# Performance work log

Hardware: AMD Instinct MI355X
Metric: run time of the kernel (lower is better)

## Reference

```python
import jax, jax.numpy as jnp
import numpy as np

LOCAL_RADIUS = 127          # block_len = 128
TOKENS_PER_BLOCK = 16       # global_seq_len = L // 16
NEG = -1e9


def _concat_3_blocks(x):
    # x: [B, nb, bl, H, d] -> [B, nb, 3*bl, H, d] (prev, cur, next block; zero-padded ends)
    p = jnp.pad(x, [(0, 0), (1, 1), (0, 0), (0, 0), (0, 0)])
    return jnp.concatenate([p[:, :-2], p[:, 1:-1], p[:, 2:]], axis=2)


def _softmax_with_extra_logit(x, axis=-1):
    m = jnp.maximum(jax.lax.stop_gradient(x.max(axis, keepdims=True)), 0)
    unnorm = jnp.exp(x - m)
    denom = unnorm.sum(axis, keepdims=True) + jnp.exp(-m)
    return unnorm / denom


def setup_inputs() -> dict:
    key = jax.random.key(0)
    ks = jax.random.split(key, 5)
    B, L, D, H, dh = 2, 4096, 1024, 16, 64
    return {
        "x": jax.random.normal(ks[0], (B, L, D), jnp.float32),
        "Wq": jax.random.normal(ks[1], (D, H, dh), jnp.float32) * 0.02,
        "Wk": jax.random.normal(ks[2], (D, H, dh), jnp.float32) * 0.02,
        "Wv": jax.random.normal(ks[3], (D, H, dh), jnp.float32) * 0.02,
        "Wo": jax.random.normal(ks[4], (H, dh, D), jnp.float32) * 0.02,
    }


def reference(x, Wq, Wk, Wv, Wo):
    B, L, D = x.shape
    H, dh = Wq.shape[1], Wq.shape[2]
    bl = LOCAL_RADIUS + 1                      # block_len = 128
    nb = L // bl                               # num_blocks
    G = L // TOKENS_PER_BLOCK                  # global (side) seq len

    q = jnp.einsum("bld,dhk->blhk", x, Wq) / jnp.sqrt(jnp.asarray(dh, x.dtype))
    k = jnp.einsum("bld,dhk->blhk", x, Wk)
    v = jnp.einsum("bld,dhk->blhk", x, Wv)

    # transient-global aggregates: sum token embeddings within each block of TOKENS_PER_BLOCK
    block_ids = jnp.arange(L) // TOKENS_PER_BLOCK          # [L]
    one_hot = jax.nn.one_hot(block_ids, G, dtype=x.dtype)  # [L, G]
    g = jnp.einsum("bld,lg->bgd", x, one_hot)              # [B, G, D]
    side_k = jnp.einsum("bgd,dhk->bghk", g, Wk)
    side_v = jnp.einsum("bgd,dhk->bghk", g, Wv)

    # split into blocks and build 3-block sliding window keys/values
    qb = q.reshape(B, nb, bl, H, dh)
    kb = _concat_3_blocks(k.reshape(B, nb, bl, H, dh))     # [B, nb, 3bl, H, dh]
    vb = _concat_3_blocks(v.reshape(B, nb, bl, H, dh))

    k_cat = jnp.concatenate(
        [kb, jnp.broadcast_to(side_k[:, None], (B, nb, G, H, dh))], axis=2)
    v_cat = jnp.concatenate(
        [vb, jnp.broadcast_to(side_v[:, None], (B, nb, G, H, dh))], axis=2)

    # logits: [B, nb, H, bl, 3bl+G]
    logits = jnp.einsum("bnqhd,bnkhd->bnhqk", qb, k_cat)

    # local mask: enforce |rel| <= local_radius and in-bounds key positions
    q_idx = jnp.arange(bl)[:, None]                        # [bl, 1]
    k_idx = jnp.arange(3 * bl)[None, :]                    # [1, 3bl]
    rel = k_idx - bl - q_idx                               # relative position
    b_idx = jnp.arange(nb)[:, None, None]                  # [nb, 1, 1]
    k_pos = (b_idx - 1) * bl + k_idx                       # absolute key position
    valid = (jnp.abs(rel) <= LOCAL_RADIUS) & (k_pos >= 0) & (k_pos < L)
    local_bias = jnp.where(valid, 0.0, NEG).astype(logits.dtype)  # [nb, bl, 3bl]
    side_bias = jnp.zeros((nb, bl, G), logits.dtype)
    bias = jnp.concatenate([local_bias, side_bias], axis=-1)      # [nb, bl, 3bl+G]
    logits = logits + bias[None, :, None]

    probs = _softmax_with_extra_logit(logits, axis=-1)
    y = jnp.einsum("bnhqk,bnkhd->bnqhd", probs, v_cat)
    y = y.reshape(B, L, H, dh)
    return jnp.einsum("blhk,hkd->bld", y, Wo)
```

## Files before the change

kernel.cpp:

```cpp
#include <hip/hip_runtime.h>
#include <stdint.h>

#define SC_LOG2E 0.18033688011112042f

typedef __attribute__((ext_vector_type(8))) short short8;
typedef __attribute__((ext_vector_type(4))) float f32x4;

__device__ __forceinline__ unsigned short f2bf(float f) {
  unsigned int u = __float_as_uint(f);
  u += 0x7fffu + ((u >> 16) & 1u);
  return (unsigned short)(u >> 16);
}

__device__ __forceinline__ void gload_lds16(const void* g, void* l) {
  __builtin_amdgcn_global_load_lds((const __attribute__((address_space(1))) void*)g,
                                   (__attribute__((address_space(3))) void*)l,
                                   16, 0, 0);
}

__device__ __forceinline__ f32x4 mfma16(short8 a, short8 b, f32x4 c) {
  return __builtin_amdgcn_mfma_f32_16x16x32_bf16(a, b, c, 0, 0, 0);
}


__global__ __launch_bounds__(256) void prep_x_k(const float* __restrict__ x,
                                                unsigned short* __restrict__ xb,
                                                unsigned short* __restrict__ gb) {
  int gr = blockIdx.x;
  int c4 = threadIdx.x;
  const float4* p = (const float4*)(x + (size_t)gr * 16384) + c4;
  float4 s = {0.f, 0.f, 0.f, 0.f};
#pragma unroll
  for (int t = 0; t < 16; ++t) {
    float4 v = p[(size_t)t * 256];
    ushort4 o;
    o.x = f2bf(v.x); o.y = f2bf(v.y); o.z = f2bf(v.z); o.w = f2bf(v.w);
    ((ushort4*)xb)[(size_t)(gr * 16 + t) * 256 + c4] = o;
    s.x += v.x; s.y += v.y; s.z += v.z; s.w += v.w;
  }
  ushort4 og;
  og.x = f2bf(s.x); og.y = f2bf(s.y); og.z = f2bf(s.z); og.w = f2bf(s.w);
  ((ushort4*)gb)[(size_t)gr * 256 + c4] = og;
}

__global__ __launch_bounds__(256) void transpose_w4_k(
    const float* __restrict__ wq, const float* __restrict__ wk,
    const float* __restrict__ wv, const float* __restrict__ wo,
    unsigned short* __restrict__ wqkv_t, unsigned short* __restrict__ wo_t) {
  __shared__ float tile[64 * 65];
  int z = blockIdx.z;
  const float* src = (z == 0) ? wq : (z == 1) ? wk : (z == 2) ? wv : wo;
  unsigned short* dst = (z == 3) ? wo_t : (wqkv_t + (size_t)z * 1048576);
  float scale = (z == 0) ? SC_LOG2E : 1.0f;
  int tc = blockIdx.x * 64, tr = blockIdx.y * 64;
  int cx = threadIdx.x & 63, ry = threadIdx.x >> 6;
#pragma unroll
  for (int i = 0; i < 16; ++i) {
    int r = ry + i * 4;
    tile[r * 65 + cx] = src[(size_t)(tr + r) * 1024 + tc + cx];
  }
  __syncthreads();
#pragma unroll
  for (int i = 0; i < 16; ++i) {
    int r = ry + i * 4;
    dst[(size_t)(tc + r) * 1024 + tr + cx] = f2bf(tile[cx * 65 + r] * scale);
  }
}

__global__ __launch_bounds__(256) void transpose_bf16_k(
    const unsigned short* __restrict__ src, int sstride, size_t szstride,
    unsigned short* __restrict__ dst, int dstride, size_t dzstride) {
  __shared__ unsigned short tile[64 * 65];
  src += blockIdx.z * szstride;
  dst += blockIdx.z * dzstride;
  int tc = blockIdx.x * 64, tr = blockIdx.y * 64;
  int cx = threadIdx.x & 63, ry = threadIdx.x >> 6;
#pragma unroll
  for (int i = 0; i < 16; ++i) {
    int r = ry + i * 4;
    tile[r * 65 + cx] = src[(size_t)(tr + r) * sstride + tc + cx];
  }
  __syncthreads();
#pragma unroll
  for (int i = 0; i < 16; ++i) {
    int r = ry + i * 4;
    dst[(size_t)(tc + r) * dstride + tr + cx] = tile[cx * 65 + r];
  }
}

__global__ __launch_bounds__(512, 2) void gemm256_k(
    const unsigned short* __restrict__ A, const unsigned short* __restrict__ Bt,
    unsigned short* __restrict__ C, int M, int N, int K, int nbn) {
  __shared__ unsigned short lds[2][2][16384];
  int nwg = gridDim.x, cpx = nwg >> 3;
  int bid = blockIdx.x;
  bid = (bid & 7) * cpx + (bid >> 3);
  int bm = bid / nbn, bn = bid % nbn;
  int lane = threadIdx.x & 63, w = threadIdx.x >> 6;
  int wm = w >> 2, wn = w & 3;
  int l15 = lane & 15, lg = lane >> 4;
  int lrow = lane >> 3;
  int lcol = ((lane & 7) ^ lrow) * 8;
  const int KT = K >> 6;

  const unsigned short* Ab = A + ((size_t)bm * 256 + lrow) * K + lcol;
  const unsigned short* Bb = Bt + ((size_t)bn * 256 + lrow) * K + lcol;

  f32x4 zero4 = {0.f, 0.f, 0.f, 0.f};
  f32x4 acc[8][4];
#pragma unroll
  for (int i = 0; i < 8; ++i)
#pragma unroll
    for (int j = 0; j < 4; ++j) acc[i][j] = zero4;

  auto stage = [&](int kind, int t) {
    if (t >= KT) return;
    const unsigned short* src = (kind < 2) ? Ab : Bb;
#pragma unroll
    for (int i = 0; i < 2; ++i) {
      int q = i * 64 + w * 8;
      int r0;
      if (kind == 0)      r0 = (q & 63) + ((q >> 6) << 7);
      else if (kind == 1) r0 = (q & 63) + ((q >> 6) << 7) + 64;
      else if (kind == 2) r0 = (q & 31) + ((q >> 5) << 6);
      else                r0 = (q & 31) + ((q >> 5) << 6) + 32;
      gload_lds16(src + (size_t)r0 * K + t * 64,
                  &lds[t & 1][kind < 2 ? 0 : 1][r0 * 64]);
    }
  };
  auto ldA = [&](int p, int mi, int kk) -> short8 {
    int r = wm * 128 + mi * 16 + l15;
    return *(const short8*)&lds[p][0][r * 64 + ((kk * 32 + lg * 8) ^ ((r & 7) * 8))];
  };
  auto ldB = [&](int p, int ni, int kk) -> short8 {
    int r = wn * 64 + ni * 16 + l15;
    return *(const short8*)&lds[p][1][r * 64 + ((kk * 32 + lg * 8) ^ ((r & 7) * 8))];
  };

  stage(0, 0); stage(3, 0); stage(1, 0); stage(2, 0);
  stage(0, 1); stage(3, 1); stage(1, 1);
  asm volatile("s_waitcnt vmcnt(6)" ::: "memory");
  __builtin_amdgcn_s_barrier();

  for (int t = 0; t < KT; ++t) {
    int p = t & 1;
    short8 aF[4][2], b0[2][2], b1[2][2];
#pragma unroll
    for (int mi = 0; mi < 4; ++mi)
#pragma unroll
      for (int kk = 0; kk < 2; ++kk) aF[mi][kk] = ldA(p, mi, kk);
#pragma unroll
    for (int ni = 0; ni < 2; ++ni)
#pragma unroll
      for (int kk = 0; kk < 2; ++kk) b0[ni][kk] = ldB(p, ni, kk);
    stage(2, t + 1);
    __builtin_amdgcn_s_barrier();
    __builtin_amdgcn_s_setprio(1);
#pragma unroll
    for (int mi = 0; mi < 4; ++mi)
#pragma unroll
      for (int ni = 0; ni < 2; ++ni)
#pragma unroll
        for (int kk = 0; kk < 2; ++kk)
          acc[mi][ni] = mfma16(aF[mi][kk], b0[ni][kk], acc[mi][ni]);
    __builtin_amdgcn_s_setprio(0);
    __builtin_amdgcn_s_barrier();
#pragma unroll
    for (int ni = 0; ni < 2; ++ni)
#pragma unroll
      for (int kk = 0; kk < 2; ++kk) b1[ni][kk] = ldB(p, ni + 2, kk);
    stage(0, t + 2);
    __builtin_amdgcn_s_barrier();
    __builtin_amdgcn_s_setprio(1);
#pragma unroll
    for (int mi = 0; mi < 4; ++mi)
#pragma unroll
      for (int ni = 0; ni < 2; ++ni)
#pragma unroll
        for (int kk = 0; kk < 2; ++kk)
          acc[mi][ni + 2] = mfma16(aF[mi][kk], b1[ni][kk], acc[mi][ni + 2]);
    __builtin_amdgcn_s_setprio(0);
    __builtin_amdgcn_s_barrier();
#pragma unroll
    for (int mi = 0; mi < 4; ++mi)
#pragma unroll
      for (int kk = 0; kk < 2; ++kk) aF[mi][kk] = ldA(p, mi + 4, kk);
    stage(3, t + 2);
    __builtin_amdgcn_s_barrier();
    __builtin_amdgcn_s_setprio(1);
#pragma unroll
    for (int mi = 0; mi < 4; ++mi)
#pragma unroll
      for (int ni = 0; ni < 2; ++ni)
#pragma unroll
        for (int kk = 0; kk < 2; ++kk)
          acc[mi + 4][ni + 2] = mfma16(aF[mi][kk], b1[ni][kk], acc[mi + 4][ni + 2]);
    __builtin_amdgcn_s_setprio(0);
    __builtin_amdgcn_s_barrier();
    stage(1, t + 2);
    if (t < KT - 2)
      asm volatile("s_waitcnt vmcnt(6)" ::: "memory");
    else
      asm volatile("s_waitcnt vmcnt(0)" ::: "memory");
    __builtin_amdgcn_s_barrier();
    __builtin_amdgcn_s_setprio(1);
#pragma unroll
    for (int mi = 0; mi < 4; ++mi)
#pragma unroll
      for (int ni = 0; ni < 2; ++ni)
#pragma unroll
        for (int kk = 0; kk < 2; ++kk)
          acc[mi + 4][ni] = mfma16(aF[mi][kk], b0[ni][kk], acc[mi + 4][ni]);
    __builtin_amdgcn_s_setprio(0);
    __builtin_amdgcn_s_barrier();
  }

#pragma unroll
  for (int mi = 0; mi < 8; ++mi) {
    size_t row = (size_t)bm * 256 + wm * 128 + mi * 16 + lg * 4;
#pragma unroll
    for (int ni = 0; ni < 4; ++ni) {
      size_t col = (size_t)bn * 256 + wn * 64 + ni * 16 + l15;
#pragma unroll
      for (int r = 0; r < 4; ++r)
        C[(row + r) * N + col] = f2bf(acc[mi][ni][r]);
    }
  }
}

template <bool F32OUT>
__global__ __launch_bounds__(256) void gemm_bt_k(
    const unsigned short* __restrict__ A, const unsigned short* __restrict__ Bt,
    void* __restrict__ Cv, int M, int N, int K, int nbn) {
  __shared__ unsigned short Alds[128 * 64];
  __shared__ unsigned short Blds[128 * 64];
  int bid = blockIdx.x;
  int bm = bid / nbn, bn = bid % nbn;
  int lane = threadIdx.x & 63, wid = threadIdx.x >> 6;
  int wr = wid >> 1, wc = wid & 1;
  int l15 = lane & 15, lg = lane >> 4;

  f32x4 zero4 = {0.f, 0.f, 0.f, 0.f};
  f32x4 acc[4][4];
#pragma unroll
  for (int i = 0; i < 4; ++i)
#pragma unroll
    for (int j = 0; j < 4; ++j) acc[i][j] = zero4;

  int srow[4], scol[4];
#pragma unroll
  for (int i = 0; i < 4; ++i) {
    int seg = wid * 4 + i;
    int r = seg * 8 + (lane >> 3);
    srow[i] = r;
    scol[i] = ((lane & 7) ^ (r & 7)) * 8;
  }
  size_t arow0 = (size_t)bm * 128, brow0 = (size_t)bn * 128;

  int ksteps = K >> 6;
  for (int ks = 0; ks < ksteps; ++ks) {
    int k0 = ks << 6;
#pragma unroll
    for (int i = 0; i < 4; ++i) {
      gload_lds16(A + (arow0 + srow[i]) * K + k0 + scol[i],
                  (char*)Alds + (wid * 4 + i) * 1024);
      gload_lds16(Bt + (brow0 + srow[i]) * K + k0 + scol[i],
                  (char*)Blds + (wid * 4 + i) * 1024);
    }
    __syncthreads();
#pragma unroll
    for (int kk = 0; kk < 2; ++kk) {
      short8 af[4], bfr[4];
#pragma unroll
      for (int mi = 0; mi < 4; ++mi) {
        int r = wr * 64 + mi * 16 + l15;
        af[mi] = *(const short8*)((const char*)Alds + r * 128 +
                                  ((kk * 64 + lg * 16) ^ ((r & 7) << 4)));
      }
#pragma unroll
      for (int ni = 0; ni < 4; ++ni) {
        int r = wc * 64 + ni * 16 + l15;
        bfr[ni] = *(const short8*)((const char*)Blds + r * 128 +
                                   ((kk * 64 + lg * 16) ^ ((r & 7) << 4)));
      }
#pragma unroll
      for (int mi = 0; mi < 4; ++mi)
#pragma unroll
        for (int ni = 0; ni < 4; ++ni)
          acc[mi][ni] = mfma16(af[mi], bfr[ni], acc[mi][ni]);
    }
    __syncthreads();
  }
  int rq = lg << 2;
#pragma unroll
  for (int mi = 0; mi < 4; ++mi) {
    size_t row = arow0 + wr * 64 + mi * 16 + rq;
#pragma unroll
    for (int ni = 0; ni < 4; ++ni) {
      size_t col = brow0 + wc * 64 + ni * 16 + l15;
#pragma unroll
      for (int r = 0; r < 4; ++r) {
        if (F32OUT)
          ((float*)Cv)[(row + r) * N + col] = acc[mi][ni][r];
        else
          ((unsigned short*)Cv)[(row + r) * N + col] = f2bf(acc[mi][ni][r]);
      }
    }
  }
}

__global__ __launch_bounds__(256) void attn_k(
    const unsigned short* __restrict__ qkv,
    const unsigned short* __restrict__ v_t,
    const unsigned short* __restrict__ side_v_t,
    unsigned short* __restrict__ y) {
  const int L = 4096, G = 256;
  __shared__ unsigned short K0[4096], V0[4096];
  __shared__ unsigned short K1[4096], V1[4096];
  __shared__ unsigned short Pl[4][2048];

  int bid = blockIdx.x;
  int n = bid & 31, h = (bid >> 5) & 15, b = bid >> 9;
  int lane = threadIdx.x & 63, wid = threadIdx.x >> 6;
  int l15 = lane & 15, lg = lane >> 4, rq = lg << 2;

  short8 qf[2][2];
  {
    size_t rowb = (size_t)b * L + n * 128 + wid * 32;
#pragma unroll
    for (int qt = 0; qt < 2; ++qt)
#pragma unroll
      for (int kk = 0; kk < 2; ++kk)
        qf[qt][kk] = *(const short8*)(qkv + (rowb + qt * 16 + l15) * 3072 +
                                      h * 64 + kk * 32 + lg * 8);
  }

  f32x4 zero4 = {0.f, 0.f, 0.f, 0.f};
  f32x4 accO[2][4], accSum[2];
#pragma unroll
  for (int qt = 0; qt < 2; ++qt) {
    accSum[qt] = zero4;
#pragma unroll
    for (int dt = 0; dt < 4; ++dt) accO[qt][dt] = zero4;
  }

  short8 onesf;
  {
    short o = (l15 == 0) ? (short)0x3F80 : (short)0;
    onesf = (short8){o, o, o, o, o, o, o, o};
  }

  int clo = (n == 0) ? 2 : 0, chi = (n == 31) ? 4 : 6;
  int nloc = chi - clo, goff = 6 - nloc;
  int m = nloc + 4;
  unsigned short* pw = Pl[wid];

  auto stage = [&](int c, unsigned short* Kl, unsigned short* Vl) {
    bool isg = c >= 6;
#pragma unroll
    for (int i = 0; i < 2; ++i) {
      int seg = wid * 2 + i;
      int r = seg * 8 + (lane >> 3);
      int sl = ((lane & 7) ^ (r & 7)) * 8;
      const unsigned short *ksrc, *vsrc;
      if (!isg) {
        int p0 = (n - 1) * 128 + c * 64;
        ksrc = qkv + (size_t)(b * L + p0 + r) * 3072 + 1024 + h * 64 + sl;
        vsrc = v_t + ((size_t)b * 1024 + h * 64 + r) * L + p0 + sl;
      } else {
        int g0 = (c - 6) * 64;
        ksrc = qkv + (size_t)(8192 + b * G + g0 + r) * 3072 + 1024 + h * 64 + sl;
        vsrc = side_v_t + ((size_t)b * 1024 + h * 64 + r) * G + g0 + sl;
      }
      gload_lds16(ksrc, (char*)Kl + seg * 1024);
      gload_lds16(vsrc, (char*)Vl + seg * 1024);
    }
  };

  auto compute = [&](int c, const unsigned short* Kl, const unsigned short* Vl) {
    bool isg = c >= 6;
    int d0 = c * 64 - 128 - wid * 32;
    if (!isg) {
      if (d0 >= 159 || d0 <= -191) return;
    }
    bool partial = !isg && !(d0 >= -96 && d0 <= 64);

    f32x4 sacc[2][4];
#pragma unroll
    for (int qt = 0; qt < 2; ++qt)
#pragma unroll
      for (int kt = 0; kt < 4; ++kt) sacc[qt][kt] = zero4;
    __builtin_amdgcn_s_setprio(1);
#pragma unroll
    for (int kk = 0; kk < 2; ++kk) {
      short8 kf[4];
#pragma unroll
      for (int kt = 0; kt < 4; ++kt) {
        int r = kt * 16 + l15;
        kf[kt] = *(const short8*)((const char*)Kl + r * 128 +
                                  ((kk * 64 + lg * 16) ^ ((r & 7) << 4)));
      }
#pragma unroll
      for (int qt = 0; qt < 2; ++qt)
#pragma unroll
        for (int kt = 0; kt < 4; ++kt)
          sacc[qt][kt] = mfma16(qf[qt][kk], kf[kt], sacc[qt][kt]);
    }
    __builtin_amdgcn_s_setprio(0);
    if (partial) {
      int relc = d0 + l15 - rq;
#pragma unroll
      for (int qt = 0; qt < 2; ++qt)
#pragma unroll
        for (int kt = 0; kt < 4; ++kt)
#pragma unroll
          for (int r = 0; r < 4; ++r) {
            int rel = relc + kt * 16 - qt * 16 - r;
            sacc[qt][kt][r] =
                ((unsigned)(rel + 127) <= 254u) ? sacc[qt][kt][r] : -1e30f;
          }
    }
#pragma unroll
    for (int qt = 0; qt < 2; ++qt)
#pragma unroll
      for (int kt = 0; kt < 4; ++kt)
#pragma unroll
        for (int r = 0; r < 4; ++r) {
          float p = __builtin_amdgcn_exp2f(sacc[qt][kt][r]);
          int row = qt * 16 + rq + r;
          int cb = (kt * 16 + l15) * 2;
          *(unsigned short*)((char*)pw + row * 128 +
                             (cb ^ ((row & 7) << 4))) = f2bf(p);
        }
    __builtin_amdgcn_s_setprio(1);
#pragma unroll
    for (int ks = 0; ks < 2; ++ks) {
      short8 pa[2], vb[4];
#pragma unroll
      for (int qt = 0; qt < 2; ++qt) {
        int row = qt * 16 + l15;
        pa[qt] = *(const short8*)((const char*)pw + row * 128 +
                                  ((ks * 64 + lg * 16) ^ ((row & 7) << 4)));
      }
#pragma unroll
      for (int dt = 0; dt < 4; ++dt) {
        int d = dt * 16 + l15;
        vb[dt] = *(const short8*)((const char*)Vl + d * 128 +
                                  ((ks * 64 + lg * 16) ^ ((d & 7) << 4)));
      }
#pragma unroll
      for (int qt = 0; qt < 2; ++qt) {
#pragma unroll
        for (int dt = 0; dt < 4; ++dt)
          accO[qt][dt] = mfma16(pa[qt], vb[dt], accO[qt][dt]);
        accSum[qt] = mfma16(pa[qt], onesf, accSum[qt]);
      }
    }
    __builtin_amdgcn_s_setprio(0);
  };

  auto chunk_of = [&](int i) { return i < nloc ? i + clo : i + goff; };

  stage(chunk_of(0), K0, V0);
  __syncthreads();
  for (int i = 0; i < m; i += 2) {
    if (i + 1 < m) stage(chunk_of(i + 1), K1, V1);
    compute(chunk_of(i), K0, V0);
    __syncthreads();
    if (i + 1 >= m) break;
    if (i + 2 < m) stage(chunk_of(i + 2), K0, V0);
    compute(chunk_of(i + 1), K1, V1);
    __syncthreads();
  }

  size_t rowb = (size_t)b * L + n * 128 + wid * 32;
#pragma unroll
  for (int qt = 0; qt < 2; ++qt) {
    float inv[4];
#pragma unroll
    for (int r = 0; r < 4; ++r) {
      float s = __shfl(accSum[qt][r], lane & 48);
      inv[r] = 1.f / (1.f + s);
    }
#pragma unroll
    for (int dt = 0; dt < 4; ++dt) {
      int col = h * 64 + dt * 16 + l15;
#pragma unroll
      for (int r = 0; r < 4; ++r)
        y[(rowb + qt * 16 + rq + r) * 1024 + col] =
            f2bf(accO[qt][dt][r] * inv[r]);
    }
  }
}

extern "C" void kernel_launch(void* const* d_in, const int* in_sizes, int n_in,
                              void* d_out, int out_size, void* d_ws, size_t ws_size,
                              hipStream_t stream) {
  const float* x  = (const float*)d_in[0];
  const float* wq = (const float*)d_in[1];
  const float* wk = (const float*)d_in[2];
  const float* wv = (const float*)d_in[3];
  const float* wo = (const float*)d_in[4];
  char* ws = (char*)d_ws;
  const size_t MB = 1 << 20;
  unsigned short* xb     = (unsigned short*)(ws);
  unsigned short* gb     = (unsigned short*)(ws + 16 * MB);
  unsigned short* wqkv_t = (unsigned short*)(ws + 17 * MB);
  unsigned short* wo_t   = (unsigned short*)(ws + 23 * MB);
  unsigned short* qkvb   = (unsigned short*)(ws + 25 * MB);
  unsigned short* vt     = (unsigned short*)(ws + 76 * MB);
  unsigned short* svt    = gb;
  unsigned short* yb     = xb;

  prep_x_k<<<512, 256, 0, stream>>>(x, xb, gb);
  transpose_w4_k<<<dim3(16, 16, 4), 256, 0, stream>>>(wq, wk, wv, wo, wqkv_t, wo_t);
  gemm256_k<<<34 * 12, 512, 0, stream>>>(xb, wqkv_t, qkvb, 8704, 3072, 1024, 12);
  transpose_bf16_k<<<dim3(16, 64, 2), 256, 0, stream>>>(
      qkvb + 2048, 3072, (size_t)4096 * 3072, vt, 4096, (size_t)1024 * 4096);
  transpose_bf16_k<<<dim3(16, 4, 2), 256, 0, stream>>>(
      qkvb + (size_t)8192 * 3072 + 2048, 3072, (size_t)256 * 3072, svt, 256,
      (size_t)1024 * 256);
  attn_k<<<1024, 256, 0, stream>>>(qkvb, vt, svt, yb);
  gemm_bt_k<true><<<64 * 8, 256, 0, stream>>>(yb, wo_t, d_out, 8192, 1024, 1024, 8);
}
```

Baseline: 162.1 us.

## Restructure GEMM main loop into two phases with hoisted swizzled LDS offsets

```diff
diff --git a/kernel.cpp b/kernel.cpp
--- a/kernel.cpp
+++ b/kernel.cpp
@@ -106,6 +106,13 @@
   const unsigned short* Ab = A + ((size_t)bm * 256 + lrow) * K + lcol;
   const unsigned short* Bb = Bt + ((size_t)bn * 256 + lrow) * K + lcol;
 
+  int x0 = 2 * ((lg * 8) ^ ((l15 & 7) * 8));
+  int x1 = 2 * ((32 | (lg * 8)) ^ ((l15 & 7) * 8));
+  int aoff0 = (wm * 128 + l15) * 128 + x0;
+  int aoff1 = (wm * 128 + l15) * 128 + x1;
+  int boff0 = (wn * 64 + l15) * 128 + x0;
+  int boff1 = (wn * 64 + l15) * 128 + x1;
+
   f32x4 zero4 = {0.f, 0.f, 0.f, 0.f};
   f32x4 acc[8][4];
 #pragma unroll
@@ -128,89 +135,61 @@
                   &lds[t & 1][kind < 2 ? 0 : 1][r0 * 64]);
     }
   };
-  auto ldA = [&](int p, int mi, int kk) -> short8 {
-    int r = wm * 128 + mi * 16 + l15;
-    return *(const short8*)&lds[p][0][r * 64 + ((kk * 32 + lg * 8) ^ ((r & 7) * 8))];
-  };
-  auto ldB = [&](int p, int ni, int kk) -> short8 {
-    int r = wn * 64 + ni * 16 + l15;
-    return *(const short8*)&lds[p][1][r * 64 + ((kk * 32 + lg * 8) ^ ((r & 7) * 8))];
-  };
-
-  stage(0, 0); stage(3, 0); stage(1, 0); stage(2, 0);
-  stage(0, 1); stage(3, 1); stage(1, 1);
+
+  stage(0, 0); stage(2, 0); stage(3, 0); stage(1, 0);
+  stage(0, 1); stage(2, 1); stage(3, 1);
   asm volatile("s_waitcnt vmcnt(6)" ::: "memory");
   __builtin_amdgcn_s_barrier();
 
   for (int t = 0; t < KT; ++t) {
-    int p = t & 1;
-    short8 aF[4][2], b0[2][2], b1[2][2];
-#pragma unroll
-    for (int mi = 0; mi < 4; ++mi)
-#pragma unroll
-      for (int kk = 0; kk < 2; ++kk) aF[mi][kk] = ldA(p, mi, kk);
-#pragma unroll
-    for (int ni = 0; ni < 2; ++ni)
-#pragma unroll
-      for (int kk = 0; kk < 2; ++kk) b0[ni][kk] = ldB(p, ni, kk);
-    stage(2, t + 1);
-    __builtin_amdgcn_s_barrier();
-    __builtin_amdgcn_s_setprio(1);
-#pragma unroll
-    for (int mi = 0; mi < 4; ++mi)
-#pragma unroll
-      for (int ni = 0; ni < 2; ++ni)
-#pragma unroll
-        for (int kk = 0; kk < 2; ++kk)
-          acc[mi][ni] = mfma16(aF[mi][kk], b0[ni][kk], acc[mi][ni]);
-    __builtin_amdgcn_s_setprio(0);
-    __builtin_amdgcn_s_barrier();
-#pragma unroll
-    for (int ni = 0; ni < 2; ++ni)
-#pragma unroll
-      for (int kk = 0; kk < 2; ++kk) b1[ni][kk] = ldB(p, ni + 2, kk);
-    stage(0, t + 2);
-    __builtin_amdgcn_s_barrier();
-    __builtin_amdgcn_s_setprio(1);
-#pragma unroll
-    for (int mi = 0; mi < 4; ++mi)
-#pragma unroll
-      for (int ni = 0; ni < 2; ++ni)
-#pragma unroll
-        for (int kk = 0; kk < 2; ++kk)
-          acc[mi][ni + 2] = mfma16(aF[mi][kk], b1[ni][kk], acc[mi][ni + 2]);
-    __builtin_amdgcn_s_setprio(0);
-    __builtin_amdgcn_s_barrier();
-#pragma unroll
-    for (int mi = 0; mi < 4; ++mi)
-#pragma unroll
-      for (int kk = 0; kk < 2; ++kk) aF[mi][kk] = ldA(p, mi + 4, kk);
-    stage(3, t + 2);
-    __builtin_amdgcn_s_barrier();
-    __builtin_amdgcn_s_setprio(1);
-#pragma unroll
-    for (int mi = 0; mi < 4; ++mi)
-#pragma unroll
-      for (int ni = 0; ni < 2; ++ni)
-#pragma unroll
-        for (int kk = 0; kk < 2; ++kk)
-          acc[mi + 4][ni + 2] = mfma16(aF[mi][kk], b1[ni][kk], acc[mi + 4][ni + 2]);
-    __builtin_amdgcn_s_setprio(0);
-    __builtin_amdgcn_s_barrier();
-    stage(1, t + 2);
+    const char* bufA = (const char*)&lds[t & 1][0][0];
+    const char* bufB = (const char*)&lds[t & 1][1][0];
+    short8 aF[4][2], bF[4][2];
+#pragma unroll
+    for (int mi = 0; mi < 4; ++mi) {
+      aF[mi][0] = *(const short8*)(bufA + aoff0 + mi * 2048);
+      aF[mi][1] = *(const short8*)(bufA + aoff1 + mi * 2048);
+    }
+#pragma unroll
+    for (int ni = 0; ni < 4; ++ni) {
+      bF[ni][0] = *(const short8*)(bufB + boff0 + ni * 2048);
+      bF[ni][1] = *(const short8*)(bufB + boff1 + ni * 2048);
+    }
+    stage(1, t + 1);
     if (t < KT - 2)
-      asm volatile("s_waitcnt vmcnt(6)" ::: "memory");
+      asm volatile("s_waitcnt vmcnt(8)" ::: "memory");
     else
       asm volatile("s_waitcnt vmcnt(0)" ::: "memory");
     __builtin_amdgcn_s_barrier();
     __builtin_amdgcn_s_setprio(1);
 #pragma unroll
-    for (int mi = 0; mi < 4; ++mi)
-#pragma unroll
-      for (int ni = 0; ni < 2; ++ni)
-#pragma unroll
-        for (int kk = 0; kk < 2; ++kk)
-          acc[mi + 4][ni] = mfma16(aF[mi][kk], b0[ni][kk], acc[mi + 4][ni]);
+    for (int kk = 0; kk < 2; ++kk)
+#pragma unroll
+      for (int mi = 0; mi < 4; ++mi)
+#pragma unroll
+        for (int ni = 0; ni < 4; ++ni)
+          acc[mi][ni] = mfma16(aF[mi][kk], bF[ni][kk], acc[mi][ni]);
+    __builtin_amdgcn_s_setprio(0);
+    __builtin_amdgcn_s_barrier();
+#pragma unroll
+    for (int mi = 0; mi < 4; ++mi) {
+      aF[mi][0] = *(const short8*)(bufA + aoff0 + (mi + 4) * 2048);
+      aF[mi][1] = *(const short8*)(bufA + aoff1 + (mi + 4) * 2048);
+    }
+    stage(0, t + 2); stage(2, t + 2); stage(3, t + 2);
+    if (t < KT - 2)
+      asm volatile("s_waitcnt vmcnt(8)" ::: "memory");
+    else
+      asm volatile("s_waitcnt vmcnt(0)" ::: "memory");
+    __builtin_amdgcn_s_barrier();
+    __builtin_amdgcn_s_setprio(1);
+#pragma unroll
+    for (int kk = 0; kk < 2; ++kk)
+#pragma unroll
+      for (int mi = 0; mi < 4; ++mi)
+#pragma unroll
+        for (int ni = 0; ni < 4; ++ni)
+          acc[mi + 4][ni] = mfma16(aF[mi][kk], bF[ni][kk], acc[mi + 4][ni]);
     __builtin_amdgcn_s_setprio(0);
     __builtin_amdgcn_s_barrier();
   }
```

Result: no change. 165.0 us (+1.8%).
